# Kernel optimization log

Hardware: AMD Instinct MI355X
Metric: run time of the kernel (lower is better)

Reference implementation:

```python
import jax, jax.numpy as jnp
import numpy as np

B, S, E = 4, 2048, 1024
H, D = 16, 64  # n_heads, head_dim; scale hardcoded as 1/sqrt(64) in source


def setup_inputs() -> dict:
    key = jax.random.key(0)
    ks = jax.random.split(key, 6)
    mk = lambda k, shp, scale=1.0: (jax.random.normal(k, shp, dtype=jnp.float32) * scale)
    return {
        "queries": mk(ks[0], (B, S, E)),
        "keys": mk(ks[1], (B, S, E)),
        "values": mk(ks[2], (B, S, E)),
        "Wq": mk(ks[3], (E, H * D), E ** -0.5),
        "Wk": mk(ks[4], (E, H * D), E ** -0.5),
        "Wv": mk(ks[5], (E, H * D), E ** -0.5),
    }


def reference(queries, keys, values, Wq, Wk, Wv):
    # linear projections
    q = jnp.einsum("bse,ef->bsf", queries, Wq).reshape(B, S, H, D)
    k = jnp.einsum("bse,ef->bsf", keys, Wk).reshape(B, S, H, D)
    v = jnp.einsum("bse,ef->bsf", values, Wv).reshape(B, S, H, D)
    # scaled dot-product attention per head (scale hardcoded to 1/sqrt(64) in source)
    scores = jnp.einsum("bqhd,bkhd->bhqk", q, k) * (1.0 / np.sqrt(64.0)).astype(np.float32)
    weights = jax.nn.softmax(scores, axis=-1)
    ctx = jnp.einsum("bhqk,bkhd->bqhd", weights, v)
    # merge heads back: [B, S, H*D]
    return ctx.reshape(B, S, H * D)
```

## Files before the change

### kernel.cpp

```cpp
#include <hip/hip_runtime.h>
#include <math.h>

#define SEQ 2048
#define EMB 1024
#define NH 16
#define HD 64
#define BH 64
#define L2E 1.44269504088896340736f

typedef __attribute__((ext_vector_type(8))) short bf16x8;
typedef __attribute__((ext_vector_type(4))) float f32x4;
typedef __attribute__((ext_vector_type(16))) float f32x16;
typedef __attribute__((ext_vector_type(4))) unsigned short u16x4;

__device__ __forceinline__ unsigned short f2bf(float f) {
  union { float fv; unsigned u; } v; v.fv = f;
  return (unsigned short)((v.u + 0x7FFFu + ((v.u >> 16) & 1u)) >> 16);
}

__device__ __forceinline__ unsigned cvt_pk_bf16(float lo, float hi) {
  unsigned r;
  asm("v_cvt_pk_bf16_f32 %0, %1, %2" : "=v"(r) : "v"(lo), "v"(hi));
  return r;
}

__device__ __forceinline__ void gl_lds16(const void* g, void* l) {
  __builtin_amdgcn_global_load_lds(
      (const __attribute__((address_space(1))) unsigned*)g,
      (__attribute__((address_space(3))) unsigned*)l, 16, 0, 0);
}

__global__ __launch_bounds__(256) void k_wt3(const float* __restrict__ Wq,
                                             const float* __restrict__ Wk,
                                             const float* __restrict__ Wv,
                                             unsigned short* __restrict__ tq,
                                             unsigned short* __restrict__ tk,
                                             unsigned short* __restrict__ tv) {
  int z = blockIdx.z;
  const float* W = (z == 0) ? Wq : (z == 1) ? Wk : Wv;
  unsigned short* Wt = (z == 0) ? tq : (z == 1) ? tk : tv;
  const float scale = (z == 0) ? 0.125f * L2E : 1.0f;

  __shared__ float tile[32][33];
  int j0 = blockIdx.x * 32, i0 = blockIdx.y * 32;
  int tx = threadIdx.x & 31, ty = threadIdx.x >> 5;
#pragma unroll
  for (int r = 0; r < 32; r += 8)
    tile[ty + r][tx] = W[(i0 + ty + r) * EMB + j0 + tx];
  __syncthreads();
#pragma unroll
  for (int r = 0; r < 32; r += 8)
    Wt[(j0 + ty + r) * EMB + i0 + tx] = f2bf(tile[tx][ty + r] * scale);
}

__global__ __launch_bounds__(256) void k_proj(
    const float* __restrict__ xq, const float* __restrict__ xk,
    const float* __restrict__ xv,
    const unsigned short* __restrict__ w0, const unsigned short* __restrict__ w1,
    const unsigned short* __restrict__ w2,
    unsigned short* __restrict__ o0, unsigned short* __restrict__ o1,
    unsigned short* __restrict__ o2) {
  int z = blockIdx.z;
  const float* X = (z == 0) ? xq : (z == 1) ? xk : xv;
  const unsigned short* Wt = (z == 0) ? w0 : (z == 1) ? w1 : w2;
  unsigned short* O = (z == 0) ? o0 : (z == 1) ? o1 : o2;

  __shared__ __align__(16) unsigned short As[2][128 * 64];
  __shared__ __align__(16) unsigned short Bs[2][128 * 64];

  int tid = threadIdx.x;
  int lane = tid & 63, w = tid >> 6;
  int ln15 = lane & 15, lg = lane >> 4;
  int wr = w >> 1, wc = w & 1;
  int row0 = blockIdx.x * 128, col0 = blockIdx.y * 128;

  const char* Xb = (const char*)X;
  const char* Wb = (const char*)Wt;

  f32x4 acc[4][4];
#pragma unroll
  for (int i = 0; i < 4; ++i)
#pragma unroll
    for (int j = 0; j < 4; ++j) acc[i][j] = (f32x4){0.f, 0.f, 0.f, 0.f};

  int oc[4], dswz[4];
  size_t srcA[4];
#pragma unroll
  for (int c = 0; c < 4; ++c) {
    oc[c] = w * 4096 + c * 1024 + lane * 16;
    dswz[c] = oc[c] ^ (((oc[c] >> 7) & 7) << 4);
    srcA[c] = (size_t)(row0 + (oc[c] >> 7)) * (EMB * 4) + (size_t)(oc[c] & 127) * 2;
  }
  int soB[4];
#pragma unroll
  for (int c = 0; c < 4; ++c) soB[c] = oc[c] ^ (((oc[c] >> 7) & 7) << 4);

  f32x4 arA[4][2], arB[4][2];
  auto ldA_A = [&](int kt) {
#pragma unroll
    for (int c = 0; c < 4; ++c) {
      const char* p = Xb + srcA[c] + kt * 256;
      arA[c][0] = *(const f32x4*)p;
      arA[c][1] = *(const f32x4*)(p + 16);
    }
  };
  auto ldA_B = [&](int kt) {
#pragma unroll
    for (int c = 0; c < 4; ++c) {
      const char* p = Xb + srcA[c] + kt * 256;
      arB[c][0] = *(const f32x4*)p;
      arB[c][1] = *(const f32x4*)(p + 16);
    }
  };
  auto wrA_A = [&](int buf) {
#pragma unroll
    for (int c = 0; c < 4; ++c) {
      union { unsigned u[4]; bf16x8 v; } pk;
      pk.u[0] = cvt_pk_bf16(arA[c][0][0], arA[c][0][1]);
      pk.u[1] = cvt_pk_bf16(arA[c][0][2], arA[c][0][3]);
      pk.u[2] = cvt_pk_bf16(arA[c][1][0], arA[c][1][1]);
      pk.u[3] = cvt_pk_bf16(arA[c][1][2], arA[c][1][3]);
      *(bf16x8*)((char*)As[buf] + dswz[c]) = pk.v;
    }
  };
  auto wrA_B = [&](int buf) {
#pragma unroll
    for (int c = 0; c < 4; ++c) {
      union { unsigned u[4]; bf16x8 v; } pk;
      pk.u[0] = cvt_pk_bf16(arB[c][0][0], arB[c][0][1]);
      pk.u[1] = cvt_pk_bf16(arB[c][0][2], arB[c][0][3]);
      pk.u[2] = cvt_pk_bf16(arB[c][1][0], arB[c][1][1]);
      pk.u[3] = cvt_pk_bf16(arB[c][1][2], arB[c][1][3]);
      *(bf16x8*)((char*)As[buf] + dswz[c]) = pk.v;
    }
  };
  auto stageB = [&](int buf, int kt) {
#pragma unroll
    for (int c = 0; c < 4; ++c)
      gl_lds16(Wb + (size_t)(col0 + (soB[c] >> 7)) * (EMB * 2) + kt * 128 + (soB[c] & 127),
               (char*)Bs[buf] + w * 4096 + c * 1024);
  };

  auto mfmaStep = [&](int cur) {
#pragma unroll
    for (int ks = 0; ks < 2; ++ks) {
      bf16x8 a[4], bb[4];
#pragma unroll
      for (int i = 0; i < 4; ++i) {
        int row = wr * 64 + i * 16 + ln15;
        int ba = (row * 128 + ks * 64 + lg * 16) ^ ((row & 7) << 4);
        a[i] = *(const bf16x8*)((const char*)As[cur] + ba);
      }
#pragma unroll
      for (int j = 0; j < 4; ++j) {
        int row = wc * 64 + j * 16 + ln15;
        int ba = (row * 128 + ks * 64 + lg * 16) ^ ((row & 7) << 4);
        bb[j] = *(const bf16x8*)((const char*)Bs[cur] + ba);
      }
      __builtin_amdgcn_s_setprio(1);
#pragma unroll
      for (int i = 0; i < 4; ++i)
#pragma unroll
        for (int j = 0; j < 4; ++j)
          acc[i][j] = __builtin_amdgcn_mfma_f32_16x16x32_bf16(a[i], bb[j], acc[i][j], 0, 0, 0);
      __builtin_amdgcn_s_setprio(0);
    }
  };

  ldA_A(0);
  stageB(0, 0);
  wrA_A(0);
  ldA_B(1);
  __syncthreads();

#pragma unroll
  for (int kp = 0; kp < 8; ++kp) {
    const int kte = 2 * kp;
    stageB(1, kte + 1);
    if (kte < 14) ldA_A(kte + 2);
    mfmaStep(0);
    wrA_B(1);
    __syncthreads();

    const int kto = 2 * kp + 1;
    if (kto < 15) stageB(0, kto + 1);
    if (kto < 14) ldA_B(kto + 2);
    mfmaStep(1);
    if (kto < 15) wrA_A(0);
    __syncthreads();
  }

  if (z == 2) {
#pragma unroll
    for (int i = 0; i < 4; ++i) {
#pragma unroll
      for (int j = 0; j < 4; ++j) {
        int col = col0 + wc * 64 + j * 16 + ln15;
        int h = col >> 6, d = col & 63;
        int rowb = row0 + wr * 64 + i * 16 + lg * 4;
        int b = rowb >> 11, s = rowb & (SEQ - 1);
        u16x4 hv;
#pragma unroll
        for (int r = 0; r < 4; ++r) hv[r] = f2bf(acc[i][j][r]);
        *(u16x4*)&O[(((size_t)(b * NH + h) * HD) + d) * SEQ + s] = hv;
      }
    }
  } else {
#pragma unroll
    for (int i = 0; i < 4; ++i) {
#pragma unroll
      for (int j = 0; j < 4; ++j) {
#pragma unroll
        for (int r = 0; r < 4; ++r) {
          int row = row0 + wr * 64 + i * 16 + lg * 4 + r;
          int col = col0 + wc * 64 + j * 16 + ln15;
          int b = row >> 11, s = row & (SEQ - 1);
          int h = col >> 6, d = col & 63;
          O[(((size_t)(b * NH + h) * SEQ) + s) * HD + d] = f2bf(acc[i][j][r]);
        }
      }
    }
  }
}

__global__ __launch_bounds__(512) void k_attn(const unsigned short* __restrict__ Q,
                                              const unsigned short* __restrict__ K,
                                              const unsigned short* __restrict__ Vt,
                                              float* __restrict__ out) {
  __shared__ __align__(16) unsigned short Klds[2 * 32 * 64];
  __shared__ __align__(16) unsigned short Vlds[2 * 64 * 64];

  const int id = blockIdx.x;
  const int swz = (id & 7) * 64 + (id >> 3);
  const int bh = swz >> 3, qb = swz & 7;
  const int b = bh >> 4, h = bh & 15;

  const int tid = threadIdx.x;
  const int w = tid >> 6, lane = tid & 63;
  const int q31 = lane & 31;
  const int hi = lane >> 5;
  const int q0 = qb * 256 + w * 32;

  const unsigned short* Qb = Q + (size_t)bh * SEQ * HD;
  const char* Kb = (const char*)(K + (size_t)bh * SEQ * HD);
  const char* Vb = (const char*)(Vt + (size_t)bh * HD * SEQ);

  bf16x8 qf[4];
#pragma unroll
  for (int kk = 0; kk < 4; ++kk)
    qf[kk] = *(const bf16x8*)&Qb[(q0 + q31) * HD + kk * 16 + hi * 8];

  f32x16 ctx[2];
#pragma unroll
  for (int db = 0; db < 2; ++db)
#pragma unroll
    for (int r = 0; r < 16; ++r) ctx[db][r] = 0.f;

  f32x16 zero16;
#pragma unroll
  for (int r = 0; r < 16; ++r) zero16[r] = 0.f;
  union { unsigned u[4]; bf16x8 v; } onesf;
#pragma unroll
  for (int r = 0; r < 4; ++r) onesf.u[r] = 0x3F803F80u;
  f32x16 lsum = zero16;

  const int sw = (q31 & 7) << 4;
  int kaddr[4];
#pragma unroll
  for (int kk = 0; kk < 4; ++kk)
    kaddr[kk] = q31 * 128 + (((kk * 32) | (hi * 16)) ^ sw);
  int vaddr[2][2];
#pragma unroll
  for (int pi = 0; pi < 2; ++pi)
#pragma unroll
    for (int j = 0; j < 2; ++j)
      vaddr[pi][j] = q31 * 128 + (((pi * 64) | (j * 32) | (hi * 16)) ^ sw);

  const int o0 = w * 1024 + lane * 16;
  const int os0 = o0 ^ (((o0 >> 7) & 7) << 4);

  auto stageK = [&](int slot, int kt) {
    if (w < 4)
      gl_lds16(Kb + (size_t)kt * 4096 + os0, (char*)Klds + slot * 4096 + w * 1024);
  };
  auto stageV = [&](int slot, int vt) {
    gl_lds16(Vb + (size_t)(os0 >> 7) * (SEQ * 2) + vt * 128 + (os0 & 127),
             (char*)Vlds + slot * 8192 + w * 1024);
  };

  auto barrierC = [&]() {
    if (w < 4) asm volatile("s_waitcnt vmcnt(1)" ::: "memory");
    __builtin_amdgcn_s_barrier();
    __builtin_amdgcn_sched_barrier(0);
  };

  auto qk = [&](f32x16& sx, const char* kbase) {
    __builtin_amdgcn_s_setprio(1);
    bf16x8 kf0 = *(const bf16x8*)(kbase + kaddr[0]);
    sx = __builtin_amdgcn_mfma_f32_32x32x16_bf16(kf0, qf[0], zero16, 0, 0, 0);
#pragma unroll
    for (int kk = 1; kk < 4; ++kk) {
      bf16x8 kf = *(const bf16x8*)(kbase + kaddr[kk]);
      sx = __builtin_amdgcn_mfma_f32_32x32x16_bf16(kf, qf[kk], sx, 0, 0, 0);
    }
    __builtin_amdgcn_s_setprio(0);
  };

  auto smpv = [&](f32x16& sx, int pinIdx, int vb) {
#pragma unroll
    for (int r = 0; r < 16; ++r) sx[r] = __builtin_amdgcn_exp2f(sx[r]);

    unsigned a0 = cvt_pk_bf16(sx[0], sx[1]);
    unsigned a1 = cvt_pk_bf16(sx[2], sx[3]);
    unsigned a2 = cvt_pk_bf16(sx[4], sx[5]);
    unsigned a3 = cvt_pk_bf16(sx[6], sx[7]);
    unsigned a4 = cvt_pk_bf16(sx[8], sx[9]);
    unsigned a5 = cvt_pk_bf16(sx[10], sx[11]);
    unsigned a6 = cvt_pk_bf16(sx[12], sx[13]);
    unsigned a7 = cvt_pk_bf16(sx[14], sx[15]);
    asm volatile("v_permlane32_swap_b32 %0, %1" : "+v"(a0), "+v"(a2));
    asm volatile("v_permlane32_swap_b32 %0, %1" : "+v"(a1), "+v"(a3));
    asm volatile("v_permlane32_swap_b32 %0, %1" : "+v"(a4), "+v"(a6));
    asm volatile("v_permlane32_swap_b32 %0, %1" : "+v"(a5), "+v"(a7));
    union { unsigned u[4]; bf16x8 v; } pa_lo, pa_hi;
    pa_lo.u[0] = a0; pa_lo.u[1] = a1; pa_lo.u[2] = a2; pa_lo.u[3] = a3;
    pa_hi.u[0] = a4; pa_hi.u[1] = a5; pa_hi.u[2] = a6; pa_hi.u[3] = a7;

    const char* vbp = (const char*)Vlds + vb;
    __builtin_amdgcn_s_setprio(1);
    lsum = __builtin_amdgcn_mfma_f32_32x32x16_bf16(pa_lo.v, onesf.v, lsum, 0, 0, 0);
    lsum = __builtin_amdgcn_mfma_f32_32x32x16_bf16(pa_hi.v, onesf.v, lsum, 0, 0, 0);
#pragma unroll
    for (int db = 0; db < 2; ++db) {
      bf16x8 v0 = *(const bf16x8*)(vbp + db * 4096 + vaddr[pinIdx][0]);
      bf16x8 v1 = *(const bf16x8*)(vbp + db * 4096 + vaddr[pinIdx][1]);
      ctx[db] = __builtin_amdgcn_mfma_f32_32x32x16_bf16(pa_lo.v, v0, ctx[db], 0, 0, 0);
      ctx[db] = __builtin_amdgcn_mfma_f32_32x32x16_bf16(pa_hi.v, v1, ctx[db], 0, 0, 0);
    }
    __builtin_amdgcn_s_setprio(0);
  };

  const char* K0 = (const char*)Klds;
  const char* K1 = (const char*)Klds + 4096;
  f32x16 sA, sB;

  stageK(0, 0);
  stageV(0, 0);
  barrierC();
  qk(sA, K0);
  stageK(1, 1);
  __syncthreads();

  for (int tp = 0; tp < 31; ++tp) {
    const int vb = (tp & 1) << 13;
    qk(sB, K1);
    stageK(0, 2 * tp + 2);
    stageV((tp + 1) & 1, tp + 1);
    smpv(sA, 0, vb);
    barrierC();
    qk(sA, K0);
    stageK(1, 2 * tp + 3);
    smpv(sB, 1, vb);
    __syncthreads();
  }
  qk(sB, K1);
  smpv(sA, 0, 8192);
  smpv(sB, 1, 8192);

#pragma unroll
  for (int db = 0; db < 2; ++db) {
#pragma unroll
    for (int r = 0; r < 16; ++r) {
      int q = q0 + (r & 3) + 8 * (r >> 2) + 4 * hi;
      out[((size_t)b * SEQ + q) * (NH * HD) + h * HD + db * 32 + q31] =
          ctx[db][r] / lsum[r];
    }
  }
}

extern "C" void kernel_launch(void* const* d_in, const int* in_sizes, int n_in,
                              void* d_out, int out_size, void* d_ws, size_t ws_size,
                              hipStream_t stream) {
  (void)in_sizes; (void)n_in; (void)out_size; (void)ws_size;
  const float* queries = (const float*)d_in[0];
  const float* keys    = (const float*)d_in[1];
  const float* values  = (const float*)d_in[2];
  const float* Wq = (const float*)d_in[3];
  const float* Wk = (const float*)d_in[4];
  const float* Wv = (const float*)d_in[5];
  float* out = (float*)d_out;

  char* ws = (char*)d_ws;
  const size_t MB = 1024 * 1024;
  unsigned short* q_ws = (unsigned short*)(ws);
  unsigned short* k_ws = (unsigned short*)(ws + 16 * MB);
  unsigned short* v_ws = (unsigned short*)(ws + 32 * MB);
  unsigned short* wtq  = (unsigned short*)(ws + 48 * MB);
  unsigned short* wtk  = (unsigned short*)(ws + 50 * MB);
  unsigned short* wtv  = (unsigned short*)(ws + 52 * MB);

  k_wt3<<<dim3(32, 32, 3), 256, 0, stream>>>(Wq, Wk, Wv, wtq, wtk, wtv);
  k_proj<<<dim3(64, 8, 3), 256, 0, stream>>>(queries, keys, values,
                                             wtq, wtk, wtv, q_ws, k_ws, v_ws);
  k_attn<<<dim3(512), 512, 0, stream>>>(q_ws, k_ws, v_ws, out);
}
```

Measured before the change: 159.8 us.

## Triple-buffer projection weight tiles and relax barrier waits with partial vmcnt

Expands the shared-memory B (weight) staging in the projection GEMM from two to three slots and issues direct global-to-LDS loads two k-tiles ahead. The full __syncthreads is replaced by an explicit barrier that waits only until at most 12 vector-memory ops remain outstanding, so newer prefetches can stay in flight across the barrier. The goal is to hide global-load latency for the weight tiles behind the MFMA work. The cost is extra LDS, which may lower occupancy. The fixed vmcnt(12) assumes a set number of loads in flight, which may not hold in the tail iterations where fewer loads are issued.

```diff
diff --git a/kernel.cpp b/kernel.cpp
--- a/kernel.cpp
+++ b/kernel.cpp
@@ -66,7 +66,7 @@
   unsigned short* O = (z == 0) ? o0 : (z == 1) ? o1 : o2;
 
   __shared__ __align__(16) unsigned short As[2][128 * 64];
-  __shared__ __align__(16) unsigned short Bs[2][128 * 64];
+  __shared__ __align__(16) unsigned short Bs[3 * 128 * 64];
 
   int tid = threadIdx.x;
   int lane = tid & 63, w = tid >> 6;
@@ -134,14 +134,15 @@
       *(bf16x8*)((char*)As[buf] + dswz[c]) = pk.v;
     }
   };
-  auto stageB = [&](int buf, int kt) {
+  auto stageB = [&](int slot, int kt) {
 #pragma unroll
     for (int c = 0; c < 4; ++c)
       gl_lds16(Wb + (size_t)(col0 + (soB[c] >> 7)) * (EMB * 2) + kt * 128 + (soB[c] & 127),
-               (char*)Bs[buf] + w * 4096 + c * 1024);
-  };
-
-  auto mfmaStep = [&](int cur) {
+               (char*)Bs + slot * 16384 + w * 4096 + c * 1024);
+  };
+
+  auto mfmaStep = [&](int cur, int bslot) {
+    const char* bbase = (const char*)Bs + bslot * 16384;
 #pragma unroll
     for (int ks = 0; ks < 2; ++ks) {
       bf16x8 a[4], bb[4];
@@ -155,7 +156,7 @@
       for (int j = 0; j < 4; ++j) {
         int row = wc * 64 + j * 16 + ln15;
         int ba = (row * 128 + ks * 64 + lg * 16) ^ ((row & 7) << 4);
-        bb[j] = *(const bf16x8*)((const char*)Bs[cur] + ba);
+        bb[j] = *(const bf16x8*)(bbase + ba);
       }
       __builtin_amdgcn_s_setprio(1);
 #pragma unroll
@@ -167,27 +168,34 @@
     }
   };
 
+  auto vbar = [&]() {
+    asm volatile("s_waitcnt vmcnt(12) lgkmcnt(0)" ::: "memory");
+    __builtin_amdgcn_s_barrier();
+    __builtin_amdgcn_sched_barrier(0);
+  };
+
   ldA_A(0);
   stageB(0, 0);
+  stageB(1, 1);
   wrA_A(0);
   ldA_B(1);
-  __syncthreads();
+  vbar();
 
 #pragma unroll
   for (int kp = 0; kp < 8; ++kp) {
     const int kte = 2 * kp;
-    stageB(1, kte + 1);
+    if (kte + 2 <= 15) stageB((kte + 2) % 3, kte + 2);
     if (kte < 14) ldA_A(kte + 2);
-    mfmaStep(0);
+    mfmaStep(0, kte % 3);
     wrA_B(1);
-    __syncthreads();
+    vbar();
 
     const int kto = 2 * kp + 1;
-    if (kto < 15) stageB(0, kto + 1);
+    if (kto + 2 <= 15) stageB((kto + 2) % 3, kto + 2);
     if (kto < 14) ldA_B(kto + 2);
-    mfmaStep(1);
+    mfmaStep(1, kto % 3);
     if (kto < 15) wrA_A(0);
-    __syncthreads();
+    vbar();
   }
 
   if (z == 2) {
```

Result: no change. 159.5 us (median of 2 runs) (-0.2%).
